# Kernel optimization log

Measured on AMD Instinct MI355X. Metric: run time of the kernel, lower is better.

## Reference

```python
import jax, jax.numpy as jnp
import numpy as np

# pars (match init_kwargs)
ALPHA, BETA = 0.9, 0.8            # synaptic / membrane decay (snn.Synaptic)
THRESHOLD = 1.0
BETA_PLUS, BETA_MINUS = 0.9, 0.9  # pre / post trace decay
A_PLUS, A_MINUS = 0.008, 0.0066   # STDP learning rates
W_MIN, W_MAX = 0.0, 1.0
NUM_STEPS, INPUT_SIZE, N_NEURONS = 256, 784, 512
SPIKE_RATE = 0.1                  # Bernoulli rate for the input spike train


def setup_inputs() -> dict:
    key = jax.random.key(0)
    k1, k2 = jax.random.split(key)
    # binary pre-synaptic spike train [num_steps, input_size]
    image = (jax.random.uniform(k1, (NUM_STEPS, INPUT_SIZE)) < SPIKE_RATE).astype(jnp.float32)
    # fc.weight, clamped into [w_min, w_max] as in __init__
    W = jax.random.uniform(k2, (N_NEURONS, INPUT_SIZE), minval=W_MIN, maxval=W_MAX)
    return {"image": image, "W": W}


def reference(image, W):
    """Faithful scan over time of: Linear -> Synaptic LIF (subtract reset) ->
    post-trace update -> classic STDP weight update with clamp.
    Returns (W_rec, spk_rec, mem_rec, syn_rec, post_rec) stacked over time."""
    dtype = image.dtype
    n = W.shape[0]
    d = image.shape[1]
    syn0 = jnp.zeros((n,), dtype)
    mem0 = jnp.zeros((n,), dtype)
    spk0 = jnp.zeros((n,), dtype)   # previous spike -> reset term
    post0 = jnp.zeros((n,), dtype)  # post-synaptic trace
    pre0 = jnp.zeros((d,), dtype)   # pre-synaptic trace (generate_traces: trace[0]=0)

    def step(carry, x_t):
        syn, mem, spk_prev, post, pre_tr, Wc = carry
        # fc (no bias)
        I = Wc @ x_t                                   # [n_neurons]
        # snntorch Synaptic, reset_mechanism='subtract' (reset from prev-step mem)
        syn = ALPHA * syn + I
        mem = BETA * mem + syn - spk_prev * THRESHOLD
        spk = (mem > THRESHOLD).astype(dtype)
        # post-synaptic trace update (before STDP, as in forward)
        post = BETA_MINUS * post + spk
        # classic STDP
        ltp = A_PLUS * jnp.outer(spk, pre_tr)          # [n, d]
        ltd = A_MINUS * jnp.outer(post, x_t)           # [n, d]
        Wn = jnp.clip(Wc + ltp - ltd, W_MIN, W_MAX)
        # pre-trace recurrence: trace[t+1] = beta_plus*trace[t] + image[t]
        pre_new = BETA_PLUS * pre_tr + x_t
        return (syn, mem, spk, post, pre_new, Wn), (spk, mem, syn, post, Wn)

    _, (spk_rec, mem_rec, syn_rec, post_rec, W_rec) = jax.lax.scan(
        step, (syn0, mem0, spk0, post0, pre0, W), image)
    return W_rec, spk_rec, mem_rec, syn_rec, post_rec
```

## Files before the change

### kernel.cpp

```cpp
#include <hip/hip_runtime.h>
#include <stdint.h>

#define NUM_STEPS  256
#define INPUT_SIZE 784
#define N_NEURONS  512

__device__ __forceinline__ float bf2f(unsigned short u) {
    union { uint32_t i; float f; } v; v.i = ((uint32_t)u) << 16; return v.f;
}
__device__ __forceinline__ unsigned short f2bf(float f) {
    union { float f; uint32_t i; } v; v.f = f;
    uint32_t x = v.i;
    return (unsigned short)((x + 0x7fffu + ((x >> 16) & 1u)) >> 16);
}

template <bool F32>
__device__ __forceinline__ void ld_chunk(const void* __restrict__ base, size_t elem, float* d) {
    if constexpr (F32) {
        const float4 v = *(const float4*)((const float*)base + elem);
        d[0] = v.x; d[1] = v.y; d[2] = v.z; d[3] = v.w;
    } else {
        const ushort4 v = *(const ushort4*)((const unsigned short*)base + elem);
        d[0] = bf2f(v.x); d[1] = bf2f(v.y); d[2] = bf2f(v.z); d[3] = bf2f(v.w);
    }
}

template <bool F32>
__device__ __forceinline__ void st_chunk(void* __restrict__ base, size_t elem, const float* s) {
    if constexpr (F32) {
        *(float4*)((float*)base + elem) = make_float4(s[0], s[1], s[2], s[3]);
    } else {
        ushort4 v;
        v.x = f2bf(s[0]); v.y = f2bf(s[1]); v.z = f2bf(s[2]); v.w = f2bf(s[3]);
        *(ushort4*)((unsigned short*)base + elem) = v;
    }
}

template <bool F32>
__device__ void scan_run(const void* __restrict__ img_v,
                         const void* __restrict__ W_v,
                         void* __restrict__ out_v)
{
    const int row  = blockIdx.x;
    const int lane = threadIdx.x;
    const bool has4 = lane < 4;

    const size_t WREC = (size_t)NUM_STEPS * N_NEURONS * INPUT_SIZE;
    const size_t SREC = (size_t)NUM_STEPS * N_NEURONS;

    size_t cofs[4];
    cofs[0] = (size_t)(lane      ) * 4;
    cofs[1] = (size_t)(lane +  64) * 4;
    cofs[2] = (size_t)(lane + 128) * 4;
    cofs[3] = (size_t)(192 + lane) * 4;

    float w[4][4], p[4][4], x[4][4], xn[4][4];
    #pragma unroll
    for (int c = 0; c < 4; ++c)
        #pragma unroll
        for (int j = 0; j < 4; ++j) { w[c][j] = 0.f; p[c][j] = 0.f; x[c][j] = 0.f; xn[c][j] = 0.f; }

    {
        const size_t wbase = (size_t)row * INPUT_SIZE;
        #pragma unroll
        for (int c = 0; c < 3; ++c) ld_chunk<F32>(W_v, wbase + cofs[c], w[c]);
        if (has4) ld_chunk<F32>(W_v, wbase + cofs[3], w[3]);
        #pragma unroll
        for (int c = 0; c < 3; ++c) ld_chunk<F32>(img_v, cofs[c], x[c]);
        if (has4) ld_chunk<F32>(img_v, cofs[3], x[3]);
    }

    float syn = 0.f, mem = 0.f, spk_prev = 0.f, post = 0.f;

    for (int t = 0; t < NUM_STEPS; ++t) {
        if (t + 1 < NUM_STEPS) {
            const size_t xbase = (size_t)(t + 1) * INPUT_SIZE;
            #pragma unroll
            for (int c = 0; c < 3; ++c) ld_chunk<F32>(img_v, xbase + cofs[c], xn[c]);
            if (has4) ld_chunk<F32>(img_v, xbase + cofs[3], xn[3]);
        }

        float partial = 0.f;
        #pragma unroll
        for (int c = 0; c < 4; ++c)
            #pragma unroll
            for (int j = 0; j < 4; ++j) partial += w[c][j] * x[c][j];

        #pragma unroll
        for (int off = 1; off < 64; off <<= 1)
            partial += __shfl_xor(partial, off, 64);
        const float I = partial;

        syn = 0.9f * syn + I;
        mem = 0.8f * mem + syn - spk_prev;
        const float spk = (mem > 1.0f) ? 1.0f : 0.0f;
        post = 0.9f * post + spk;
        const float ap = 0.008f  * spk;
        const float am = 0.0066f * post;

        const size_t r     = (size_t)t * N_NEURONS + row;
        const size_t obase = r * INPUT_SIZE;

        #pragma unroll
        for (int c = 0; c < 4; ++c)
            #pragma unroll
            for (int j = 0; j < 4; ++j)
                w[c][j] = fminf(fmaxf(w[c][j] + ap * p[c][j] - am * x[c][j], 0.f), 1.f);

        #pragma unroll
        for (int c = 0; c < 3; ++c) st_chunk<F32>(out_v, obase + cofs[c], w[c]);
        if (has4) st_chunk<F32>(out_v, obase + cofs[3], w[3]);

        if (lane == 0) {
            if constexpr (F32) {
                float* out = (float*)out_v;
                out[WREC + 0 * SREC + r] = spk;
                out[WREC + 1 * SREC + r] = mem;
                out[WREC + 2 * SREC + r] = syn;
                out[WREC + 3 * SREC + r] = post;
            } else {
                unsigned short* out = (unsigned short*)out_v;
                out[WREC + 0 * SREC + r] = f2bf(spk);
                out[WREC + 1 * SREC + r] = f2bf(mem);
                out[WREC + 2 * SREC + r] = f2bf(syn);
                out[WREC + 3 * SREC + r] = f2bf(post);
            }
        }

        #pragma unroll
        for (int c = 0; c < 4; ++c)
            #pragma unroll
            for (int j = 0; j < 4; ++j) {
                p[c][j] = 0.9f * p[c][j] + x[c][j];
                x[c][j] = xn[c][j];
            }
        spk_prev = spk;
    }
}

__global__ __launch_bounds__(64) void snn_row_scan_kernel(
    const void* __restrict__ img,
    const void* __restrict__ W,
    void* __restrict__ out)
{
    const unsigned short* w16 = (const unsigned short*)W;
    bool f32 = false;
    for (int i = 0; i < 128; ++i) f32 |= (w16[i] > 0x3F80u);
    if (f32) scan_run<true >(img, W, out);
    else     scan_run<false>(img, W, out);
}

extern "C" void kernel_launch(void* const* d_in, const int* in_sizes, int n_in,
                              void* d_out, int out_size, void* d_ws, size_t ws_size,
                              hipStream_t stream) {
    (void)in_sizes; (void)n_in; (void)d_ws; (void)ws_size; (void)out_size;
    snn_row_scan_kernel<<<dim3(N_NEURONS), dim3(64), 0, stream>>>(d_in[0], d_in[1], d_out);
}
```

Before: 649.4 us.

## Bit-pack input spikes in LDS, use nontemporal stores, batch state writes

Each block now runs two rows, one per wave. At the start it packs the binary image into per-lane bitmasks in shared memory, so the time loop no longer issues global image loads. The weight-record stores become nontemporal to avoid polluting caches with the large write stream. The per-step scalar state outputs are buffered in LDS and written 64 at a time. The step is unrolled 4x with rotating register buffers. The mask encoding assumes inputs are exactly 0 or 1, which the task guarantees for binary spike trains but which would silently change results for non-binary inputs.

```diff
diff --git a/kernel.cpp b/kernel.cpp
--- a/kernel.cpp
+++ b/kernel.cpp
@@ -4,6 +4,9 @@
 #define NUM_STEPS  256
 #define INPUT_SIZE 784
 #define N_NEURONS  512
+
+typedef float    v4f __attribute__((ext_vector_type(4)));
+typedef uint16_t v4h __attribute__((ext_vector_type(4)));
 
 __device__ __forceinline__ float bf2f(unsigned short u) {
     union { uint32_t i; float f; } v; v.i = ((uint32_t)u) << 16; return v.f;
@@ -17,32 +20,36 @@
 template <bool F32>
 __device__ __forceinline__ void ld_chunk(const void* __restrict__ base, size_t elem, float* d) {
     if constexpr (F32) {
-        const float4 v = *(const float4*)((const float*)base + elem);
+        const v4f v = *(const v4f*)((const float*)base + elem);
         d[0] = v.x; d[1] = v.y; d[2] = v.z; d[3] = v.w;
     } else {
-        const ushort4 v = *(const ushort4*)((const unsigned short*)base + elem);
+        const v4h v = *(const v4h*)((const unsigned short*)base + elem);
         d[0] = bf2f(v.x); d[1] = bf2f(v.y); d[2] = bf2f(v.z); d[3] = bf2f(v.w);
     }
 }
 
 template <bool F32>
-__device__ __forceinline__ void st_chunk(void* __restrict__ base, size_t elem, const float* s) {
+__device__ __forceinline__ void st_chunk_nt(void* __restrict__ base, size_t elem, const float* s) {
     if constexpr (F32) {
-        *(float4*)((float*)base + elem) = make_float4(s[0], s[1], s[2], s[3]);
+        v4f v; v.x = s[0]; v.y = s[1]; v.z = s[2]; v.w = s[3];
+        __builtin_nontemporal_store(v, (v4f*)((float*)base + elem));
     } else {
-        ushort4 v;
-        v.x = f2bf(s[0]); v.y = f2bf(s[1]); v.z = f2bf(s[2]); v.w = f2bf(s[3]);
-        *(ushort4*)((unsigned short*)base + elem) = v;
+        v4h v; v.x = f2bf(s[0]); v.y = f2bf(s[1]); v.z = f2bf(s[2]); v.w = f2bf(s[3]);
+        __builtin_nontemporal_store(v, (v4h*)((unsigned short*)base + elem));
     }
 }
 
 template <bool F32>
 __device__ void scan_run(const void* __restrict__ img_v,
                          const void* __restrict__ W_v,
-                         void* __restrict__ out_v)
+                         void* __restrict__ out_v,
+                         uint2 (&msk)[64][64],
+                         float (&sbuf)[2][64][4])
 {
-    const int row  = blockIdx.x;
-    const int lane = threadIdx.x;
+    const int tid  = threadIdx.x;
+    const int wid  = tid >> 6;
+    const int lane = tid & 63;
+    const int row  = (blockIdx.x << 1) | wid;
     const bool has4 = lane < 4;
 
     const size_t WREC = (size_t)NUM_STEPS * N_NEURONS * INPUT_SIZE;
@@ -54,105 +61,134 @@
     cofs[2] = (size_t)(lane + 128) * 4;
     cofs[3] = (size_t)(192 + lane) * 4;
 
-    float w[4][4], p[4][4], x[4][4], xn[4][4];
+    for (int i = wid; i < 64; i += 2) {
+        uint32_t lo = 0, hi = 0;
+        #pragma unroll
+        for (int s = 0; s < 4; ++s) {
+            const int t = 4 * i + s;
+            float a[4][4] = {};
+            const size_t xb = (size_t)t * INPUT_SIZE;
+            ld_chunk<F32>(img_v, xb + cofs[0], a[0]);
+            ld_chunk<F32>(img_v, xb + cofs[1], a[1]);
+            ld_chunk<F32>(img_v, xb + cofs[2], a[2]);
+            if (has4) ld_chunk<F32>(img_v, xb + cofs[3], a[3]);
+            uint32_t m = 0;
+            #pragma unroll
+            for (int c = 0; c < 4; ++c)
+                #pragma unroll
+                for (int j = 0; j < 4; ++j)
+                    m |= (uint32_t)(a[c][j] != 0.0f) << (4 * c + j);
+            if      (s == 0) lo  = m;
+            else if (s == 1) lo |= m << 16;
+            else if (s == 2) hi  = m;
+            else             hi |= m << 16;
+        }
+        msk[i][lane] = make_uint2(lo, hi);
+    }
+
+    float wb0[16], wb1[16], wb2[16], wb3[16], p[16];
     #pragma unroll
-    for (int c = 0; c < 4; ++c)
-        #pragma unroll
-        for (int j = 0; j < 4; ++j) { w[c][j] = 0.f; p[c][j] = 0.f; x[c][j] = 0.f; xn[c][j] = 0.f; }
-
+    for (int k = 0; k < 16; ++k) { wb0[k] = 0.f; wb1[k] = 0.f; wb2[k] = 0.f; wb3[k] = 0.f; p[k] = 0.f; }
     {
         const size_t wbase = (size_t)row * INPUT_SIZE;
-        #pragma unroll
-        for (int c = 0; c < 3; ++c) ld_chunk<F32>(W_v, wbase + cofs[c], w[c]);
-        if (has4) ld_chunk<F32>(W_v, wbase + cofs[3], w[3]);
-        #pragma unroll
-        for (int c = 0; c < 3; ++c) ld_chunk<F32>(img_v, cofs[c], x[c]);
-        if (has4) ld_chunk<F32>(img_v, cofs[3], x[3]);
+        ld_chunk<F32>(W_v, wbase + cofs[0], &wb0[0]);
+        ld_chunk<F32>(W_v, wbase + cofs[1], &wb0[4]);
+        ld_chunk<F32>(W_v, wbase + cofs[2], &wb0[8]);
+        if (has4) ld_chunk<F32>(W_v, wbase + cofs[3], &wb0[12]);
     }
 
+    __syncthreads();
+
     float syn = 0.f, mem = 0.f, spk_prev = 0.f, post = 0.f;
+    int t = 0;
 
-    for (int t = 0; t < NUM_STEPS; ++t) {
-        if (t + 1 < NUM_STEPS) {
-            const size_t xbase = (size_t)(t + 1) * INPUT_SIZE;
-            #pragma unroll
-            for (int c = 0; c < 3; ++c) ld_chunk<F32>(img_v, xbase + cofs[c], xn[c]);
-            if (has4) ld_chunk<F32>(img_v, xbase + cofs[3], xn[3]);
-        }
+#define STEP(WI, WO, MB) do {                                                   \
+        const uint32_t mb_ = (MB);                                              \
+        float xf[16];                                                           \
+        _Pragma("unroll")                                                       \
+        for (int k = 0; k < 16; ++k) xf[k] = ((mb_ >> k) & 1u) ? 1.0f : 0.0f;   \
+                                        \
+        float g[8];                                                             \
+        _Pragma("unroll")                                                       \
+        for (int k = 0; k < 8; ++k)                                             \
+            g[k] = WI[2*k] * xf[2*k] + WI[2*k+1] * xf[2*k+1];                   \
+        const float h0_ = (g[0] + g[1]) + (g[2] + g[3]);                        \
+        const float h1_ = (g[4] + g[5]) + (g[6] + g[7]);                        \
+        float partial = h0_ + h1_;                                              \
+        _Pragma("unroll")                                                       \
+        for (int off = 1; off < 64; off <<= 1)                                  \
+            partial += __shfl_xor(partial, off, 64);                            \
+                       \
+        syn = 0.9f * syn + partial;                                             \
+        mem = 0.8f * mem + syn - spk_prev;                                      \
+        const float spk = (mem > 1.0f) ? 1.0f : 0.0f;                           \
+        post = 0.9f * post + spk;                                               \
+        const float ap = 0.008f * spk, am = 0.0066f * post;                     \
+        \
+        _Pragma("unroll")                                                       \
+        for (int k = 0; k < 16; ++k)                                            \
+            WO[k] = fminf(fmaxf(WI[k] + ap * p[k] - am * xf[k], 0.0f), 1.0f);   \
+        const size_t r_  = (size_t)t * N_NEURONS + row;                         \
+        const size_t ob_ = r_ * INPUT_SIZE;                                     \
+        st_chunk_nt<F32>(out_v, ob_ + cofs[0], &WO[0]);                         \
+        st_chunk_nt<F32>(out_v, ob_ + cofs[1], &WO[4]);                         \
+        st_chunk_nt<F32>(out_v, ob_ + cofs[2], &WO[8]);                         \
+        if (has4) st_chunk_nt<F32>(out_v, ob_ + cofs[3], &WO[12]);              \
+        if (lane == 0) {                                                        \
+            v4f sv_; sv_.x = spk; sv_.y = mem; sv_.z = syn; sv_.w = post;       \
+            *(v4f*)&sbuf[wid][t & 63][0] = sv_;                                 \
+        }                                                                       \
+        _Pragma("unroll")                                                       \
+        for (int k = 0; k < 16; ++k) p[k] = 0.9f * p[k] + xf[k];                \
+        spk_prev = spk; ++t;                                                    \
+    } while (0)
 
-        float partial = 0.f;
-        #pragma unroll
-        for (int c = 0; c < 4; ++c)
-            #pragma unroll
-            for (int j = 0; j < 4; ++j) partial += w[c][j] * x[c][j];
-
-        #pragma unroll
-        for (int off = 1; off < 64; off <<= 1)
-            partial += __shfl_xor(partial, off, 64);
-        const float I = partial;
-
-        syn = 0.9f * syn + I;
-        mem = 0.8f * mem + syn - spk_prev;
-        const float spk = (mem > 1.0f) ? 1.0f : 0.0f;
-        post = 0.9f * post + spk;
-        const float ap = 0.008f  * spk;
-        const float am = 0.0066f * post;
-
-        const size_t r     = (size_t)t * N_NEURONS + row;
-        const size_t obase = r * INPUT_SIZE;
-
-        #pragma unroll
-        for (int c = 0; c < 4; ++c)
-            #pragma unroll
-            for (int j = 0; j < 4; ++j)
-                w[c][j] = fminf(fmaxf(w[c][j] + ap * p[c][j] - am * x[c][j], 0.f), 1.f);
-
-        #pragma unroll
-        for (int c = 0; c < 3; ++c) st_chunk<F32>(out_v, obase + cofs[c], w[c]);
-        if (has4) st_chunk<F32>(out_v, obase + cofs[3], w[3]);
-
-        if (lane == 0) {
+    for (int i = 0; i < 64; ++i) {
+        const uint2 mp = msk[i][lane];
+        STEP(wb0, wb1, mp.x & 0xFFFFu);
+        STEP(wb1, wb2, mp.x >> 16);
+        STEP(wb2, wb3, mp.y & 0xFFFFu);
+        STEP(wb3, wb0, mp.y >> 16);
+        if ((i & 15) == 15) {
+            const int t0 = (i - 15) * 4;
+            const v4f sv = *(const v4f*)&sbuf[wid][lane][0];
+            const size_t rr = (size_t)(t0 + lane) * N_NEURONS + row;
             if constexpr (F32) {
                 float* out = (float*)out_v;
-                out[WREC + 0 * SREC + r] = spk;
-                out[WREC + 1 * SREC + r] = mem;
-                out[WREC + 2 * SREC + r] = syn;
-                out[WREC + 3 * SREC + r] = post;
+                out[WREC + 0 * SREC + rr] = sv.x;
+                out[WREC + 1 * SREC + rr] = sv.y;
+                out[WREC + 2 * SREC + rr] = sv.z;
+                out[WREC + 3 * SREC + rr] = sv.w;
             } else {
                 unsigned short* out = (unsigned short*)out_v;
-                out[WREC + 0 * SREC + r] = f2bf(spk);
-                out[WREC + 1 * SREC + r] = f2bf(mem);
-                out[WREC + 2 * SREC + r] = f2bf(syn);
-                out[WREC + 3 * SREC + r] = f2bf(post);
+                out[WREC + 0 * SREC + rr] = f2bf(sv.x);
+                out[WREC + 1 * SREC + rr] = f2bf(sv.y);
+                out[WREC + 2 * SREC + rr] = f2bf(sv.z);
+                out[WREC + 3 * SREC + rr] = f2bf(sv.w);
             }
         }
-
-        #pragma unroll
-        for (int c = 0; c < 4; ++c)
-            #pragma unroll
-            for (int j = 0; j < 4; ++j) {
-                p[c][j] = 0.9f * p[c][j] + x[c][j];
-                x[c][j] = xn[c][j];
-            }
-        spk_prev = spk;
     }
+#undef STEP
 }
 
-__global__ __launch_bounds__(64) void snn_row_scan_kernel(
+__global__ __launch_bounds__(128) void snn_row_scan_kernel(
     const void* __restrict__ img,
     const void* __restrict__ W,
     void* __restrict__ out)
 {
+    __shared__ uint2 msk[64][64];
+    __shared__ float sbuf[2][64][4];
+
     const unsigned short* w16 = (const unsigned short*)W;
     bool f32 = false;
     for (int i = 0; i < 128; ++i) f32 |= (w16[i] > 0x3F80u);
-    if (f32) scan_run<true >(img, W, out);
-    else     scan_run<false>(img, W, out);
+    if (f32) scan_run<true >(img, W, out, msk, sbuf);
+    else     scan_run<false>(img, W, out, msk, sbuf);
 }
 
 extern "C" void kernel_launch(void* const* d_in, const int* in_sizes, int n_in,
                               void* d_out, int out_size, void* d_ws, size_t ws_size,
                               hipStream_t stream) {
     (void)in_sizes; (void)n_in; (void)d_ws; (void)ws_size; (void)out_size;
-    snn_row_scan_kernel<<<dim3(N_NEURONS), dim3(64), 0, stream>>>(d_in[0], d_in[1], d_out);
+    snn_row_scan_kernel<<<dim3(N_NEURONS / 2), dim3(128), 0, stream>>>(d_in[0], d_in[1], d_out);
 }
```

Measured after the change: 557.9 us. 14.1% less time.
